# Performance work log

Hardware: AMD Instinct MI355X
Metric: run time of the kernel (lower is better)

Reference implementation:

```python
import jax, jax.numpy as jnp
import numpy as np

D_IN = 1024
D_OUT = 1024
NUM_HEADS = 16
HEAD_DIM = D_OUT // NUM_HEADS
ORDERS = 4


def setup_inputs() -> dict:
    key = jax.random.key(0)
    k_x, k_t, k_w, k_b, k_a = jax.random.split(key, 5)
    x = jax.random.normal(k_x, (8, 4096, D_IN), dtype=jnp.float32)
    t_scalar = jax.random.uniform(k_t, (), dtype=jnp.float32)
    # Linear params (torch nn.Linear: y = x @ W.T + b)
    W = jax.random.normal(k_w, (D_OUT, D_IN), dtype=jnp.float32) * (1.0 / np.sqrt(D_IN))
    b = jax.random.normal(k_b, (D_OUT,), dtype=jnp.float32) * 0.01
    A = jax.random.normal(k_a, (NUM_HEADS, HEAD_DIM, HEAD_DIM), dtype=jnp.float32) * 0.02
    return {"x": x, "t_scalar": t_scalar, "W": W, "b": b, "A": A}


def reference(x, t_scalar, W, b, A):
    # proj_in
    z = jnp.einsum('bsd,od->bso', x, W) + b  # [B, S, d_out]
    B, S, _ = z.shape
    z = z.reshape(B, S, NUM_HEADS, HEAD_DIM)
    # Taylor series: out = sum_{k=0}^{ORDERS} (t*A)^k z / k!
    out = z
    term = z
    for order in range(1, ORDERS + 1):
        term = jnp.einsum('hij,bnhj->bnhi', A, term) * (t_scalar / float(order))
        out = out + term
    return out.reshape(B, S, D_OUT)
```

## Files before the change

kernel.cpp:

```cpp
#include <hip/hip_runtime.h>
#include <hip/hip_bf16.h>
#include <cstdint>

#define NHEAD 16
#define ORDERS 4

typedef short short8 __attribute__((ext_vector_type(8)));
typedef float f32x4 __attribute__((ext_vector_type(4)));

__device__ __forceinline__ unsigned short f32_to_bf16_rtn(float f) {
  union { float f; unsigned u; } v; v.f = f;
  unsigned r = v.u + 0x7FFFu + ((v.u >> 16) & 1u);
  return (unsigned short)(r >> 16);
}

typedef __attribute__((address_space(1))) void gvoid;
typedef __attribute__((address_space(3))) void svoid;
__device__ __forceinline__ void gload_lds16(const void* g, void* l) {
  __builtin_amdgcn_global_load_lds((gvoid*)g, (svoid*)l, 16, 0, 0);
}

__global__ __launch_bounds__(256) void prologue_kernel(
    const float* __restrict__ X, const float* __restrict__ A,
    const float* __restrict__ t_ptr, const float* __restrict__ W,
    const float* __restrict__ bvec, unsigned short* __restrict__ Xb,
    unsigned short* __restrict__ Weff, float* __restrict__ beff, int n8) {
  __shared__ float Ah[64 * 65];
  __shared__ float T0[64 * 64];
  __shared__ float T1[64 * 64];

  const int tid = threadIdx.x;

  if (blockIdx.x >= 256) {
    int idx = ((int)blockIdx.x - 256) * 256 + tid;
    const int stride = 2048 * 256;
    for (int i = idx; i < n8; i += stride) {
      float4 a = *(const float4*)(X + (size_t)i * 8);
      float4 b = *(const float4*)(X + (size_t)i * 8 + 4);
      unsigned short t[8] = {f32_to_bf16_rtn(a.x), f32_to_bf16_rtn(a.y),
                             f32_to_bf16_rtn(a.z), f32_to_bf16_rtn(a.w),
                             f32_to_bf16_rtn(b.x), f32_to_bf16_rtn(b.y),
                             f32_to_bf16_rtn(b.z), f32_to_bf16_rtn(b.w)};
      *(uint4*)(Xb + (size_t)i * 8) = *(const uint4*)t;
    }
    return;
  }

  const int h = blockIdx.x >> 4;
  const int c = blockIdx.x & 15;
  const int d = tid & 63;
  const int ig = tid >> 6;

  float wreg[16];
  #pragma unroll
  for (int r = 0; r < 16; ++r)
    wreg[r] = W[(size_t)(h * 64 + ig * 16 + r) * 1024 + c * 64 + d];

  const float t = t_ptr[0];
  const int i = tid >> 2;
  const int jq = (tid & 3) << 4;

  for (int r = 0; r < 16; ++r) {
    int idx = tid + 256 * r;
    Ah[(idx >> 6) * 65 + (idx & 63)] = A[h * 4096 + idx];
  }
  float ms[16];
  #pragma unroll
  for (int cc = 0; cc < 16; ++cc) {
    float e = (i == jq + cc) ? 1.0f : 0.0f;
    T0[i * 64 + jq + cc] = e;
    ms[cc] = e;
  }
  __syncthreads();

  float* Tc = T0;
  float* Tn = T1;
  for (int k = 1; k <= ORDERS; ++k) {
    float scale = t / (float)k;
    float acc[16];
    #pragma unroll
    for (int cc = 0; cc < 16; ++cc) acc[cc] = 0.f;
    for (int l = 0; l < 64; ++l) {
      float a = Ah[i * 65 + l];
      float4 t0 = *(const float4*)&Tc[l * 64 + jq];
      float4 t1 = *(const float4*)&Tc[l * 64 + jq + 4];
      float4 t2 = *(const float4*)&Tc[l * 64 + jq + 8];
      float4 t3 = *(const float4*)&Tc[l * 64 + jq + 12];
      acc[0] += a * t0.x;  acc[1] += a * t0.y;  acc[2] += a * t0.z;  acc[3] += a * t0.w;
      acc[4] += a * t1.x;  acc[5] += a * t1.y;  acc[6] += a * t1.z;  acc[7] += a * t1.w;
      acc[8] += a * t2.x;  acc[9] += a * t2.y;  acc[10] += a * t2.z; acc[11] += a * t2.w;
      acc[12] += a * t3.x; acc[13] += a * t3.y; acc[14] += a * t3.z; acc[15] += a * t3.w;
    }
    #pragma unroll
    for (int cc = 0; cc < 16; ++cc) { acc[cc] *= scale; ms[cc] += acc[cc]; }
    #pragma unroll
    for (int u = 0; u < 4; ++u) {
      float4 v = {acc[u * 4], acc[u * 4 + 1], acc[u * 4 + 2], acc[u * 4 + 3]};
      *(float4*)&Tn[i * 64 + jq + u * 4] = v;
    }
    __syncthreads();
    float* tmp = Tc; Tc = Tn; Tn = tmp;
  }

  float* Mh = Ah;
  #pragma unroll
  for (int u = 0; u < 4; ++u) {
    float4 v = {ms[u * 4], ms[u * 4 + 1], ms[u * 4 + 2], ms[u * 4 + 3]};
    *(float4*)&Mh[i * 64 + jq + u * 4] = v;
  }
  float* Wc = T0;
  #pragma unroll
  for (int r = 0; r < 16; ++r) Wc[(ig * 16 + r) * 64 + d] = wreg[r];
  __syncthreads();

  #pragma unroll
  for (int ii = 0; ii < 16; ++ii) {
    int i2 = ig * 16 + ii;
    float acc = 0.f;
    #pragma unroll
    for (int j = 0; j < 64; ++j) acc += Mh[i2 * 64 + j] * Wc[j * 64 + d];
    Weff[(size_t)(h * 64 + i2) * 1024 + c * 64 + d] = f32_to_bf16_rtn(acc);
  }
  if (c == 0 && tid < 64) {
    float acc = 0.f;
    for (int j = 0; j < 64; ++j) acc += Mh[tid * 64 + j] * bvec[h * 64 + j];
    beff[h * 64 + tid] = acc;
  }
}

#define CSTR 132

__global__ __launch_bounds__(256, 2) void gemm_kernel(
    const unsigned short* __restrict__ Xb, const unsigned short* __restrict__ Wf,
    const float* __restrict__ beff, float* __restrict__ Out) {
  __shared__ __align__(16) unsigned short smem[4 * 8192];

  const int wg = blockIdx.x;
  const int swz = (wg & 7) * 256 + (wg >> 3);
  const int by = swz >> 3;
  const int bx = swz & 7;
  const int R = by * 128;
  const int C = bx * 128;

  const int tid = threadIdx.x;
  const int lane = tid & 63;
  const int wave = tid >> 6;
  const int wm = wave >> 1;
  const int wn = wave & 1;
  const int frow = lane & 15;
  const int fkg = lane >> 4;

  f32x4 acc[4][4];
  #pragma unroll
  for (int mi = 0; mi < 4; ++mi)
    #pragma unroll
    for (int ni = 0; ni < 4; ++ni) acc[mi][ni] = (f32x4){0.f, 0.f, 0.f, 0.f};

  const int lr = lane >> 3;
  const int lc = lane & 7;
  const int scol = ((lc ^ lr) << 3);
  const unsigned short* Asrc = Xb + (size_t)(R + wave * 32 + lr) * 1024 + scol;
  const unsigned short* Bsrc = Wf + (size_t)(C + wave * 32 + lr) * 1024 + scol;

  auto stage = [&](int kt) {
    unsigned short* base = smem + (kt & 1) * 16384;
    char* Ad = (char*)(base + wave * 32 * 64);
    char* Bd = (char*)(base + 8192 + wave * 32 * 64);
    const int kb = kt * 64;
    #pragma unroll
    for (int i = 0; i < 4; ++i)
      gload_lds16(Asrc + (size_t)(i * 8) * 1024 + kb, Ad + i * 1024);
    #pragma unroll
    for (int i = 0; i < 4; ++i)
      gload_lds16(Bsrc + (size_t)(i * 8) * 1024 + kb, Bd + i * 1024);
  };

  stage(0);
  for (int kt = 0; kt < 16; ++kt) {
    if (kt < 15) {
      stage(kt + 1);
      asm volatile("s_waitcnt vmcnt(8)" ::: "memory");
    } else {
      asm volatile("s_waitcnt vmcnt(0)" ::: "memory");
    }
    __builtin_amdgcn_sched_barrier(0);
    __builtin_amdgcn_s_barrier();

    const unsigned short* As = smem + (kt & 1) * 16384;
    const unsigned short* Bs = As + 8192;
    short8 afr[4][2], bfr[4][2];
    #pragma unroll
    for (int mi = 0; mi < 4; ++mi) {
      int ar = wm * 64 + mi * 16 + frow;
      #pragma unroll
      for (int kk = 0; kk < 2; ++kk) {
        int slot = (kk * 4 + fkg) ^ (ar & 7);
        afr[mi][kk] = *(const short8*)&As[ar * 64 + slot * 8];
      }
    }
    #pragma unroll
    for (int ni = 0; ni < 4; ++ni) {
      int br = wn * 64 + ni * 16 + frow;
      #pragma unroll
      for (int kk = 0; kk < 2; ++kk) {
        int slot = (kk * 4 + fkg) ^ (br & 7);
        bfr[ni][kk] = *(const short8*)&Bs[br * 64 + slot * 8];
      }
    }
    asm volatile("s_waitcnt lgkmcnt(0)" ::: "memory");
    __builtin_amdgcn_sched_barrier(0);
    __builtin_amdgcn_s_barrier();

    #pragma unroll
    for (int mi = 0; mi < 4; ++mi)
      #pragma unroll
      for (int ni = 0; ni < 4; ++ni)
        #pragma unroll
        for (int kk = 0; kk < 2; ++kk)
          acc[mi][ni] = __builtin_amdgcn_mfma_f32_16x16x32_bf16(
              afr[mi][kk], bfr[ni][kk], acc[mi][ni], 0, 0, 0);
  }
  __syncthreads();

  float* Cs = (float*)smem;
  const int c4 = (tid & 31) << 2;
  float4 bb = *(const float4*)&beff[C + c4];
  #pragma unroll
  for (int mi = 0; mi < 4; ++mi) {
    #pragma unroll
    for (int ni = 0; ni < 4; ++ni) {
      int col = wn * 64 + ni * 16 + frow;
      #pragma unroll
      for (int reg = 0; reg < 4; ++reg)
        Cs[(wm * 16 + fkg * 4 + reg) * CSTR + col] = acc[mi][ni][reg];
    }
    __syncthreads();
    #pragma unroll
    for (int it = 0; it < 4; ++it) {
      int rloc = it * 8 + (tid >> 5);
      float4 v = *(const float4*)&Cs[rloc * CSTR + c4];
      v.x += bb.x; v.y += bb.y; v.z += bb.z; v.w += bb.w;
      int grow = R + (rloc >> 4) * 64 + mi * 16 + (rloc & 15);
      *(float4*)(Out + (size_t)grow * 1024 + C + c4) = v;
    }
    __syncthreads();
  }
}

#define LDSS 72
#define CSTRF 136
__global__ __launch_bounds__(256, 2) void gemm_fb(
    const float* __restrict__ X, const unsigned short* __restrict__ Weff,
    const float* __restrict__ beff, float* __restrict__ Out) {
  __shared__ __align__(16) unsigned short As0[128 * LDSS];
  __shared__ __align__(16) unsigned short As1[128 * LDSS];
  __shared__ __align__(16) unsigned short Bs0[128 * LDSS];
  __shared__ __align__(16) unsigned short Bs1[128 * LDSS];
  const int wg = blockIdx.x;
  const int swz = (wg & 7) * 256 + (wg >> 3);
  const int R = (swz >> 3) * 128;
  const int C = (swz & 7) * 128;
  const int tid = threadIdx.x;
  const int lane = tid & 63;
  const int wave = tid >> 6;
  const int wm = wave >> 1, wn = wave & 1;
  const int frow = lane & 15, fkg = lane >> 4;
  f32x4 acc[4][4];
  #pragma unroll
  for (int mi = 0; mi < 4; ++mi)
    #pragma unroll
    for (int ni = 0; ni < 4; ++ni) acc[mi][ni] = (f32x4){0.f, 0.f, 0.f, 0.f};
  const int ar = tid >> 4, akc = (tid & 15) << 2;
  const int bn_ = tid >> 3, bkc = (tid & 7) << 3;
  const float* Xbase = X + (size_t)(R + ar) * 1024 + akc;
  const unsigned short* Wbase = Weff + (size_t)(C + bn_) * 1024 + bkc;
  float4 av[8];
  uint4 bv[4];
  auto loadTile = [&](int kt) {
    const int kb = kt * 64;
    #pragma unroll
    for (int i = 0; i < 8; ++i) av[i] = *(const float4*)(Xbase + (size_t)i * 16 * 1024 + kb);
    #pragma unroll
    for (int i = 0; i < 4; ++i) bv[i] = *(const uint4*)(Wbase + (size_t)i * 32 * 1024 + kb);
  };
  auto writeTile = [&](unsigned short* Asn, unsigned short* Bsn) {
    #pragma unroll
    for (int i = 0; i < 8; ++i) {
      unsigned short tmp[4] = {f32_to_bf16_rtn(av[i].x), f32_to_bf16_rtn(av[i].y),
                               f32_to_bf16_rtn(av[i].z), f32_to_bf16_rtn(av[i].w)};
      *(uint2*)&Asn[(ar + i * 16) * LDSS + akc] = *(const uint2*)tmp;
    }
    #pragma unroll
    for (int i = 0; i < 4; ++i) *(uint4*)&Bsn[(bn_ + i * 32) * LDSS + bkc] = bv[i];
  };
  loadTile(0);
  writeTile(As0, Bs0);
  __syncthreads();
  unsigned short* Asc = As0; unsigned short* Asn = As1;
  unsigned short* Bsc = Bs0; unsigned short* Bsn = Bs1;
  for (int kt = 0; kt < 16; ++kt) {
    if (kt < 15) loadTile(kt + 1);
    short8 afr[4][2], bfr[4][2];
    #pragma unroll
    for (int mi = 0; mi < 4; ++mi)
      #pragma unroll
      for (int kk = 0; kk < 2; ++kk)
        afr[mi][kk] = *(const short8*)&Asc[(wm * 64 + mi * 16 + frow) * LDSS + kk * 32 + fkg * 8];
    #pragma unroll
    for (int ni = 0; ni < 4; ++ni)
      #pragma unroll
      for (int kk = 0; kk < 2; ++kk)
        bfr[ni][kk] = *(const short8*)&Bsc[(wn * 64 + ni * 16 + frow) * LDSS + kk * 32 + fkg * 8];
    #pragma unroll
    for (int mi = 0; mi < 4; ++mi)
      #pragma unroll
      for (int ni = 0; ni < 4; ++ni)
        #pragma unroll
        for (int kk = 0; kk < 2; ++kk)
          acc[mi][ni] = __builtin_amdgcn_mfma_f32_16x16x32_bf16(
              afr[mi][kk], bfr[ni][kk], acc[mi][ni], 0, 0, 0);
    if (kt < 15) writeTile(Asn, Bsn);
    __syncthreads();
    unsigned short* t1 = Asc; Asc = Asn; Asn = t1;
    unsigned short* t2 = Bsc; Bsc = Bsn; Bsn = t2;
  }
  float* Cs = (float*)As0;
  const int c4 = (tid & 31) << 2;
  float4 bb = *(const float4*)&beff[C + c4];
  #pragma unroll
  for (int mi = 0; mi < 4; ++mi) {
    #pragma unroll
    for (int ni = 0; ni < 4; ++ni) {
      int col = wn * 64 + ni * 16 + frow;
      #pragma unroll
      for (int reg = 0; reg < 4; ++reg)
        Cs[(wm * 16 + fkg * 4 + reg) * CSTRF + col] = acc[mi][ni][reg];
    }
    __syncthreads();
    #pragma unroll
    for (int it = 0; it < 4; ++it) {
      int rloc = it * 8 + (tid >> 5);
      float4 v = *(const float4*)&Cs[rloc * CSTRF + c4];
      v.x += bb.x; v.y += bb.y; v.z += bb.z; v.w += bb.w;
      int grow = R + (rloc >> 4) * 64 + mi * 16 + (rloc & 15);
      *(float4*)(Out + (size_t)grow * 1024 + C + c4) = v;
    }
    __syncthreads();
  }
}

extern "C" void kernel_launch(void* const* d_in, const int* in_sizes, int n_in,
                              void* d_out, int out_size, void* d_ws, size_t ws_size,
                              hipStream_t stream) {
  const float* x = (const float*)d_in[0];
  const float* t = (const float*)d_in[1];
  const float* W = (const float*)d_in[2];
  const float* b = (const float*)d_in[3];
  const float* A = (const float*)d_in[4];
  float* out = (float*)d_out;

  char* ws = (char*)d_ws;
  unsigned short* Weff = (unsigned short*)ws;
  float* beff = (float*)(ws + (2 << 20));
  unsigned short* Xb = (unsigned short*)(ws + (4ull << 20));

  const size_t need = (4ull << 20) + (64ull << 20);
  if (ws_size >= need) {
    prologue_kernel<<<2304, 256, 0, stream>>>(x, A, t, W, b, Xb, Weff, beff,
                                              33554432 / 8);
    gemm_kernel<<<2048, 256, 0, stream>>>(Xb, Weff, beff, out);
  } else {
    prologue_kernel<<<256, 256, 0, stream>>>(x, A, t, W, b, Xb, Weff, beff,
                                             33554432 / 8);
    gemm_fb<<<2048, 256, 0, stream>>>(x, Weff, beff, out);
  }
}
```

Measured before the change: 154.6 us.

## Fuse fp32-to-bf16 conversion of X into GEMM A-tile loads

Removes the separate pass that converts X to bf16 into workspace. The GEMM now loads fp32 X into registers two tiles ahead, packs it to bf16 and writes it to swizzled LDS, while B still uses direct global-to-LDS loads. This drops a 128MB read and 64MB write/read round trip, at the cost of higher register pressure and more complex vmcnt accounting. The fallback kernel and workspace-size branch are removed.

```diff
diff --git a/kernel.cpp b/kernel.cpp
--- a/kernel.cpp
+++ b/kernel.cpp
@@ -14,38 +14,26 @@
   return (unsigned short)(r >> 16);
 }
 
+__device__ __forceinline__ unsigned pack2(float lo, float hi) {
+  __hip_bfloat162 h = __float22bfloat162_rn(float2{lo, hi});
+  return *reinterpret_cast<unsigned*>(&h);
+}
+
 typedef __attribute__((address_space(1))) void gvoid;
 typedef __attribute__((address_space(3))) void svoid;
 __device__ __forceinline__ void gload_lds16(const void* g, void* l) {
   __builtin_amdgcn_global_load_lds((gvoid*)g, (svoid*)l, 16, 0, 0);
 }
 
-__global__ __launch_bounds__(256) void prologue_kernel(
-    const float* __restrict__ X, const float* __restrict__ A,
-    const float* __restrict__ t_ptr, const float* __restrict__ W,
-    const float* __restrict__ bvec, unsigned short* __restrict__ Xb,
-    unsigned short* __restrict__ Weff, float* __restrict__ beff, int n8) {
+__global__ __launch_bounds__(256) void weff_kernel(
+    const float* __restrict__ A, const float* __restrict__ t_ptr,
+    const float* __restrict__ W, const float* __restrict__ bvec,
+    unsigned short* __restrict__ Weff, float* __restrict__ beff) {
   __shared__ float Ah[64 * 65];
   __shared__ float T0[64 * 64];
   __shared__ float T1[64 * 64];
 
   const int tid = threadIdx.x;
-
-  if (blockIdx.x >= 256) {
-    int idx = ((int)blockIdx.x - 256) * 256 + tid;
-    const int stride = 2048 * 256;
-    for (int i = idx; i < n8; i += stride) {
-      float4 a = *(const float4*)(X + (size_t)i * 8);
-      float4 b = *(const float4*)(X + (size_t)i * 8 + 4);
-      unsigned short t[8] = {f32_to_bf16_rtn(a.x), f32_to_bf16_rtn(a.y),
-                             f32_to_bf16_rtn(a.z), f32_to_bf16_rtn(a.w),
-                             f32_to_bf16_rtn(b.x), f32_to_bf16_rtn(b.y),
-                             f32_to_bf16_rtn(b.z), f32_to_bf16_rtn(b.w)};
-      *(uint4*)(Xb + (size_t)i * 8) = *(const uint4*)t;
-    }
-    return;
-  }
-
   const int h = blockIdx.x >> 4;
   const int c = blockIdx.x & 15;
   const int d = tid & 63;
@@ -131,16 +119,14 @@
 #define CSTR 132
 
 __global__ __launch_bounds__(256, 2) void gemm_kernel(
-    const unsigned short* __restrict__ Xb, const unsigned short* __restrict__ Wf,
+    const float* __restrict__ X, const unsigned short* __restrict__ Wf,
     const float* __restrict__ beff, float* __restrict__ Out) {
   __shared__ __align__(16) unsigned short smem[4 * 8192];
 
   const int wg = blockIdx.x;
   const int swz = (wg & 7) * 256 + (wg >> 3);
-  const int by = swz >> 3;
-  const int bx = swz & 7;
-  const int R = by * 128;
-  const int C = bx * 128;
+  const int R = (swz >> 3) * 128;
+  const int C = (swz & 7) * 128;
 
   const int tid = threadIdx.x;
   const int lane = tid & 63;
@@ -156,37 +142,66 @@
     #pragma unroll
     for (int ni = 0; ni < 4; ++ni) acc[mi][ni] = (f32x4){0.f, 0.f, 0.f, 0.f};
 
+  const int arow = tid >> 3;
+  const int aseg = tid & 7;
+  const int aslot = aseg ^ (arow & 7);
+  const float* Asrc = X + (size_t)(R + arow) * 1024 + aseg * 8;
+
   const int lr = lane >> 3;
   const int lc = lane & 7;
-  const int scol = ((lc ^ lr) << 3);
-  const unsigned short* Asrc = Xb + (size_t)(R + wave * 32 + lr) * 1024 + scol;
-  const unsigned short* Bsrc = Wf + (size_t)(C + wave * 32 + lr) * 1024 + scol;
-
-  auto stage = [&](int kt) {
-    unsigned short* base = smem + (kt & 1) * 16384;
-    char* Ad = (char*)(base + wave * 32 * 64);
-    char* Bd = (char*)(base + 8192 + wave * 32 * 64);
+  const unsigned short* Bsrc = Wf + (size_t)(C + wave * 32 + lr) * 1024 + ((lc ^ lr) << 3);
+
+  float4 aA[2][8];
+
+  auto loadA = [&](int kt) {
+    const int set = kt & 1;
     const int kb = kt * 64;
     #pragma unroll
+    for (int i = 0; i < 4; ++i) {
+      const float* p = Asrc + (size_t)(i * 32) * 1024 + kb;
+      aA[set][2 * i] = *(const float4*)p;
+      aA[set][2 * i + 1] = *(const float4*)(p + 4);
+    }
+  };
+  auto loadB = [&](int kt) {
+    unsigned short* Bd = smem + (kt & 1) * 16384 + 8192 + wave * 2048;
+    const int kb = kt * 64;
+    #pragma unroll
     for (int i = 0; i < 4; ++i)
-      gload_lds16(Asrc + (size_t)(i * 8) * 1024 + kb, Ad + i * 1024);
-    #pragma unroll
-    for (int i = 0; i < 4; ++i)
-      gload_lds16(Bsrc + (size_t)(i * 8) * 1024 + kb, Bd + i * 1024);
+      gload_lds16(Bsrc + (size_t)(i * 8) * 1024 + kb, (char*)Bd + i * 1024);
   };
-
-  stage(0);
-  for (int kt = 0; kt < 16; ++kt) {
-    if (kt < 15) {
-      stage(kt + 1);
-      asm volatile("s_waitcnt vmcnt(8)" ::: "memory");
-    } else {
-      asm volatile("s_waitcnt vmcnt(0)" ::: "memory");
-    }
+  auto writeA = [&](int kt) {
+    const int set = kt & 1;
+    unsigned short* Ad = smem + set * 16384;
+    #pragma unroll
+    for (int i = 0; i < 4; ++i) {
+      uint4 w = make_uint4(pack2(aA[set][2 * i].x, aA[set][2 * i].y),
+                           pack2(aA[set][2 * i].z, aA[set][2 * i].w),
+                           pack2(aA[set][2 * i + 1].x, aA[set][2 * i + 1].y),
+                           pack2(aA[set][2 * i + 1].z, aA[set][2 * i + 1].w));
+      *(uint4*)((char*)Ad + (arow + i * 32) * 128 + aslot * 16) = w;
+    }
+  };
+
+  loadA(0);
+  loadA(1);
+  loadB(0);
+  asm volatile("s_waitcnt vmcnt(12)" ::: "memory");
+  __builtin_amdgcn_sched_barrier(0);
+
+  #pragma unroll
+  for (int t = 0; t < 16; ++t) {
+    writeA(t);
+    if (t + 2 < 16) loadA(t + 2);
+    if (t + 1 < 16) loadB(t + 1);
+    if (t <= 13)      asm volatile("s_waitcnt vmcnt(12)" ::: "memory");
+    else if (t == 14) asm volatile("s_waitcnt vmcnt(4)" ::: "memory");
+    else              asm volatile("s_waitcnt vmcnt(0)" ::: "memory");
+    asm volatile("s_waitcnt lgkmcnt(0)" ::: "memory");
     __builtin_amdgcn_sched_barrier(0);
     __builtin_amdgcn_s_barrier();
 
-    const unsigned short* As = smem + (kt & 1) * 16384;
+    const unsigned short* As = smem + (t & 1) * 16384;
     const unsigned short* Bs = As + 8192;
     short8 afr[4][2], bfr[4][2];
     #pragma unroll
@@ -239,108 +254,6 @@
     for (int it = 0; it < 4; ++it) {
       int rloc = it * 8 + (tid >> 5);
       float4 v = *(const float4*)&Cs[rloc * CSTR + c4];
-      v.x += bb.x; v.y += bb.y; v.z += bb.z; v.w += bb.w;
-      int grow = R + (rloc >> 4) * 64 + mi * 16 + (rloc & 15);
-      *(float4*)(Out + (size_t)grow * 1024 + C + c4) = v;
-    }
-    __syncthreads();
-  }
-}
-
-#define LDSS 72
-#define CSTRF 136
-__global__ __launch_bounds__(256, 2) void gemm_fb(
-    const float* __restrict__ X, const unsigned short* __restrict__ Weff,
-    const float* __restrict__ beff, float* __restrict__ Out) {
-  __shared__ __align__(16) unsigned short As0[128 * LDSS];
-  __shared__ __align__(16) unsigned short As1[128 * LDSS];
-  __shared__ __align__(16) unsigned short Bs0[128 * LDSS];
-  __shared__ __align__(16) unsigned short Bs1[128 * LDSS];
-  const int wg = blockIdx.x;
-  const int swz = (wg & 7) * 256 + (wg >> 3);
-  const int R = (swz >> 3) * 128;
-  const int C = (swz & 7) * 128;
-  const int tid = threadIdx.x;
-  const int lane = tid & 63;
-  const int wave = tid >> 6;
-  const int wm = wave >> 1, wn = wave & 1;
-  const int frow = lane & 15, fkg = lane >> 4;
-  f32x4 acc[4][4];
-  #pragma unroll
-  for (int mi = 0; mi < 4; ++mi)
-    #pragma unroll
-    for (int ni = 0; ni < 4; ++ni) acc[mi][ni] = (f32x4){0.f, 0.f, 0.f, 0.f};
-  const int ar = tid >> 4, akc = (tid & 15) << 2;
-  const int bn_ = tid >> 3, bkc = (tid & 7) << 3;
-  const float* Xbase = X + (size_t)(R + ar) * 1024 + akc;
-  const unsigned short* Wbase = Weff + (size_t)(C + bn_) * 1024 + bkc;
-  float4 av[8];
-  uint4 bv[4];
-  auto loadTile = [&](int kt) {
-    const int kb = kt * 64;
-    #pragma unroll
-    for (int i = 0; i < 8; ++i) av[i] = *(const float4*)(Xbase + (size_t)i * 16 * 1024 + kb);
-    #pragma unroll
-    for (int i = 0; i < 4; ++i) bv[i] = *(const uint4*)(Wbase + (size_t)i * 32 * 1024 + kb);
-  };
-  auto writeTile = [&](unsigned short* Asn, unsigned short* Bsn) {
-    #pragma unroll
-    for (int i = 0; i < 8; ++i) {
-      unsigned short tmp[4] = {f32_to_bf16_rtn(av[i].x), f32_to_bf16_rtn(av[i].y),
-                               f32_to_bf16_rtn(av[i].z), f32_to_bf16_rtn(av[i].w)};
-      *(uint2*)&Asn[(ar + i * 16) * LDSS + akc] = *(const uint2*)tmp;
-    }
-    #pragma unroll
-    for (int i = 0; i < 4; ++i) *(uint4*)&Bsn[(bn_ + i * 32) * LDSS + bkc] = bv[i];
-  };
-  loadTile(0);
-  writeTile(As0, Bs0);
-  __syncthreads();
-  unsigned short* Asc = As0; unsigned short* Asn = As1;
-  unsigned short* Bsc = Bs0; unsigned short* Bsn = Bs1;
-  for (int kt = 0; kt < 16; ++kt) {
-    if (kt < 15) loadTile(kt + 1);
-    short8 afr[4][2], bfr[4][2];
-    #pragma unroll
-    for (int mi = 0; mi < 4; ++mi)
-      #pragma unroll
-      for (int kk = 0; kk < 2; ++kk)
-        afr[mi][kk] = *(const short8*)&Asc[(wm * 64 + mi * 16 + frow) * LDSS + kk * 32 + fkg * 8];
-    #pragma unroll
-    for (int ni = 0; ni < 4; ++ni)
-      #pragma unroll
-      for (int kk = 0; kk < 2; ++kk)
-        bfr[ni][kk] = *(const short8*)&Bsc[(wn * 64 + ni * 16 + frow) * LDSS + kk * 32 + fkg * 8];
-    #pragma unroll
-    for (int mi = 0; mi < 4; ++mi)
-      #pragma unroll
-      for (int ni = 0; ni < 4; ++ni)
-        #pragma unroll
-        for (int kk = 0; kk < 2; ++kk)
-          acc[mi][ni] = __builtin_amdgcn_mfma_f32_16x16x32_bf16(
-              afr[mi][kk], bfr[ni][kk], acc[mi][ni], 0, 0, 0);
-    if (kt < 15) writeTile(Asn, Bsn);
-    __syncthreads();
-    unsigned short* t1 = Asc; Asc = Asn; Asn = t1;
-    unsigned short* t2 = Bsc; Bsc = Bsn; Bsn = t2;
-  }
-  float* Cs = (float*)As0;
-  const int c4 = (tid & 31) << 2;
-  float4 bb = *(const float4*)&beff[C + c4];
-  #pragma unroll
-  for (int mi = 0; mi < 4; ++mi) {
-    #pragma unroll
-    for (int ni = 0; ni < 4; ++ni) {
-      int col = wn * 64 + ni * 16 + frow;
-      #pragma unroll
-      for (int reg = 0; reg < 4; ++reg)
-        Cs[(wm * 16 + fkg * 4 + reg) * CSTRF + col] = acc[mi][ni][reg];
-    }
-    __syncthreads();
-    #pragma unroll
-    for (int it = 0; it < 4; ++it) {
-      int rloc = it * 8 + (tid >> 5);
-      float4 v = *(const float4*)&Cs[rloc * CSTRF + c4];
       v.x += bb.x; v.y += bb.y; v.z += bb.z; v.w += bb.w;
       int grow = R + (rloc >> 4) * 64 + mi * 16 + (rloc & 15);
       *(float4*)(Out + (size_t)grow * 1024 + C + c4) = v;
@@ -362,16 +275,7 @@
   char* ws = (char*)d_ws;
   unsigned short* Weff = (unsigned short*)ws;
   float* beff = (float*)(ws + (2 << 20));
-  unsigned short* Xb = (unsigned short*)(ws + (4ull << 20));
-
-  const size_t need = (4ull << 20) + (64ull << 20);
-  if (ws_size >= need) {
-    prologue_kernel<<<2304, 256, 0, stream>>>(x, A, t, W, b, Xb, Weff, beff,
-                                              33554432 / 8);
-    gemm_kernel<<<2048, 256, 0, stream>>>(Xb, Weff, beff, out);
-  } else {
-    prologue_kernel<<<256, 256, 0, stream>>>(x, A, t, W, b, Xb, Weff, beff,
-                                             33554432 / 8);
-    gemm_fb<<<2048, 256, 0, stream>>>(x, Weff, beff, out);
-  }
-}
+
+  weff_kernel<<<256, 256, 0, stream>>>(A, t, W, b, Weff, beff);
+  gemm_kernel<<<2048, 256, 0, stream>>>(x, Weff, beff, out);
+}
```

Result: slower. 162.7 us (+5.2%).
